# Kernel tuning notes

Measured on AMD Instinct MI355X. Metric: run time of the kernel, lower is better.

Reference implementation:

```python
import jax, jax.numpy as jnp
import numpy as np

EPS = 1e-6  # config.eps


def setup_inputs() -> dict:
    key = jax.random.key(0)
    k1, k2, k3, k4, k5 = jax.random.split(key, 5)
    B, Lq, Lk, D, Dc = 4, 2048, 4096, 1024, 512
    # scale so Poincare-ball norms stay < 1 (realistic hyperbolic embeddings)
    q = jax.random.normal(k1, (B, Lq, D), dtype=jnp.float32) * 0.01
    k_compressed = jax.random.randint(k2, (B, Lk, Dc), 0, 16, dtype=jnp.int32)  # 4-bit codes
    # up-projection weight, torch Linear layout (out=D, in=Dc)
    W_up = jax.random.normal(k3, (D, Dc), dtype=jnp.float32) / np.sqrt(Dc)
    k_scale = jax.random.uniform(k4, (B, Lk, 1), dtype=jnp.float32) * 0.005
    k_zero = jax.random.uniform(k5, (B, Lk, 1), dtype=jnp.float32) * 16.0
    return {"q": q, "k_compressed": k_compressed, "W_up": W_up,
            "k_scale": k_scale, "k_zero": k_zero}


def reference(q, k_compressed, W_up, k_scale, k_zero):
    # dequantize: (B, Lk, Dc)
    kc = k_scale * (k_compressed.astype(jnp.float32) - k_zero)
    # decompress: (B, Lk, D)  --  Linear(Dc -> D), y = x @ W_up.T
    k = jnp.einsum('bkc,dc->bkd', kc, W_up)

    q_sq = jnp.sum(q * q, axis=-1)   # (B, Lq) raw squared norms
    k_sq = jnp.sum(k * k, axis=-1)   # (B, Lk)

    # ||q - k||^2 via algebraic expansion (avoids (B,Lq,Lk,D) diff tensor)
    cross = jnp.einsum('bqd,bkd->bqk', q, k)                 # (B, Lq, Lk)
    diff_norm_sq = jnp.maximum(q_sq[:, :, None] + k_sq[:, None, :] - 2.0 * cross, 0.0)

    # clamped norms used in the Poincare denominator
    q_cl = jnp.minimum(q_sq, 1.0 - EPS)
    k_cl = jnp.minimum(k_sq, 1.0 - EPS)
    denom = (1.0 - q_cl)[:, :, None] * (1.0 - k_cl)[:, None, :] + EPS

    dist = jnp.arccosh(1.0 + 2.0 * diff_norm_sq / denom)     # (B, Lq, Lk)
    return dist
```

## Files before the change

kernel.cpp:

```cpp
#include <hip/hip_runtime.h>
#include <hip/hip_bf16.h>
#include <stdint.h>

typedef unsigned short u16;

#define B_  4
#define LQ  2048
#define LK  4096
#define D_  1024
#define DC  512
#define EPSF 1e-6f

typedef __bf16 bf16x8 __attribute__((ext_vector_type(8)));
typedef float  f32x4  __attribute__((ext_vector_type(4)));

__device__ __forceinline__ u16 f2bf(float f) {
    uint32_t u = __float_as_uint(f);
    uint32_t r = (u + 0x7FFFu + ((u >> 16) & 1u)) >> 16;
    return (u16)r;
}
__device__ __forceinline__ float bf2f(u16 h) {
    return __uint_as_float(((uint32_t)h) << 16);
}
__device__ __forceinline__ void gload_lds16(const void* g, void* l) {
    __builtin_amdgcn_global_load_lds(
        (const __attribute__((address_space(1))) uint32_t*)g,
        (__attribute__((address_space(3))) uint32_t*)l, 16, 0, 0);
}

#define NB_Q2  2048
#define NB_WT  ((D_ / 64) * (DC / 64))
#define NB_WS  4
#define NB_DQ2 4096

__global__ void prep_all(const float* __restrict__ q, u16* __restrict__ qb,
                         float* __restrict__ qsq,
                         const float* __restrict__ w, u16* __restrict__ wth,
                         u16* __restrict__ wtl, float* __restrict__ partS,
                         const int* __restrict__ kc, const float* __restrict__ scale,
                         const float* __restrict__ zero, u16* __restrict__ codeb,
                         u16* __restrict__ kcb) {
    __shared__ float t[64][65];
    __shared__ float red[4];
    const int bid = blockIdx.x;
    const int tid = threadIdx.x;

    if (bid < NB_Q2) {
        int row = bid * 4 + (tid >> 6);
        int ln = tid & 63;
        const float4* qr = reinterpret_cast<const float4*>(q + (size_t)row * D_);
        ushort4* ob = reinterpret_cast<ushort4*>(qb + (size_t)row * D_);
        float s = 0.f;
        #pragma unroll
        for (int c = 0; c < 4; c++) {
            float4 v = qr[c * 64 + ln];
            ushort4 o;
            o.x = f2bf(v.x); o.y = f2bf(v.y); o.z = f2bf(v.z); o.w = f2bf(v.w);
            ob[c * 64 + ln] = o;
            s += v.x * v.x + v.y * v.y + v.z * v.z + v.w * v.w;
        }
        #pragma unroll
        for (int off = 32; off; off >>= 1) s += __shfl_down(s, off);
        if (ln == 0) qsq[row] = s;
    } else if (bid < NB_Q2 + NB_WT) {
        int b2 = bid - NB_Q2;
        int d0 = (b2 % (D_ / 64)) * 64, c0 = (b2 / (D_ / 64)) * 64;
        int tx = tid & 15, ty = tid >> 4;
        #pragma unroll
        for (int r = 0; r < 4; r++) {
            float4 v = *reinterpret_cast<const float4*>(&w[(size_t)(d0 + ty + r * 16) * DC + c0 + tx * 4]);
            t[ty + r * 16][tx * 4 + 0] = v.x;
            t[ty + r * 16][tx * 4 + 1] = v.y;
            t[ty + r * 16][tx * 4 + 2] = v.z;
            t[ty + r * 16][tx * 4 + 3] = v.w;
        }
        __syncthreads();
        #pragma unroll
        for (int r = 0; r < 4; r++) {
            int c = c0 + ty + r * 16;
            ushort4 h, l;
            float v0 = t[tx * 4 + 0][ty + r * 16];
            float v1 = t[tx * 4 + 1][ty + r * 16];
            float v2 = t[tx * 4 + 2][ty + r * 16];
            float v3 = t[tx * 4 + 3][ty + r * 16];
            h.x = f2bf(v0); l.x = f2bf(v0 - bf2f(h.x));
            h.y = f2bf(v1); l.y = f2bf(v1 - bf2f(h.y));
            h.z = f2bf(v2); l.z = f2bf(v2 - bf2f(h.z));
            h.w = f2bf(v3); l.w = f2bf(v3 - bf2f(h.w));
            *reinterpret_cast<ushort4*>(&wth[(size_t)c * D_ + d0 + tx * 4]) = h;
            *reinterpret_cast<ushort4*>(&wtl[(size_t)c * D_ + d0 + tx * 4]) = l;
        }
    } else if (bid < NB_Q2 + NB_WT + NB_WS) {
        int b2 = bid - NB_Q2 - NB_WT;
        int d = b2 * 256 + tid;
        const float4* row = reinterpret_cast<const float4*>(w + (size_t)d * DC);
        float u = 0.f;
        #pragma unroll 8
        for (int i = 0; i < DC / 4; i++) { float4 v = row[i]; u += v.x + v.y + v.z + v.w; }
        float p = u * u;
        #pragma unroll
        for (int off = 32; off; off >>= 1) p += __shfl_down(p, off);
        if ((tid & 63) == 0) red[tid >> 6] = p;
        __syncthreads();
        if (tid == 0) partS[b2] = red[0] + red[1] + red[2] + red[3];
    } else {
        int row = (bid - NB_Q2 - NB_WT - NB_WS) * 4 + (tid >> 6);
        int ln = tid & 63;
        float sc = scale[row], z = zero[row];
        const int2* src = reinterpret_cast<const int2*>(kc + (size_t)row * DC);
        ushort2* dc = reinterpret_cast<ushort2*>(codeb + (size_t)row * DC);
        ushort2* dk = reinterpret_cast<ushort2*>(kcb + (size_t)row * DC);
        #pragma unroll
        for (int c = 0; c < 4; c++) {
            int2 v = src[c * 64 + ln];
            ushort2 cb, kb;
            cb.x = f2bf((float)v.x);
            cb.y = f2bf((float)v.y);
            kb.x = f2bf(sc * ((float)v.x - z));
            kb.y = f2bf(sc * ((float)v.y - z));
            dc[c * 64 + ln] = cb;
            dk[c * 64 + ln] = kb;
        }
    }
}

__global__ __launch_bounds__(256, 2) void gemm_gq(const u16* __restrict__ Wth,
                                                  const u16* __restrict__ Wtl,
                                                  float* __restrict__ gp,
                                                  const u16* __restrict__ Q,
                                                  u16* __restrict__ Cq) {
    __shared__ u16 smem[4][128 * 32];
    const int tid = threadIdx.x;
    const int wid = tid >> 6, lane = tid & 63;
    const int lr = lane & 15, lk = lane >> 4;
    const int wr = wid >> 1, wc = wid & 1;
    const int srow = tid >> 2;
    const int scol = (tid & 3) * 8;

    if (blockIdx.x < 64) {
        const int t = blockIdx.x >> 2, s = blockIdx.x & 3;
        const int m0 = (t & 3) * 128, n0 = (t >> 2) * 128;
        const int K = D_;
        f32x4 acc[4][4] = {};
        const size_t gA = (size_t)(m0 + srow) * K + scol;
        const size_t gB = (size_t)(n0 + srow) * K + scol;
        char* ashb = (char*)(&smem[0][0]) + (wid << 10);
        char* aslb = (char*)(&smem[1][0]) + (wid << 10);
        char* bshb = (char*)(&smem[2][0]) + (wid << 10);
        char* bslb = (char*)(&smem[3][0]) + (wid << 10);

        for (int k0 = s * 256; k0 < s * 256 + 256; k0 += 32) {
            gload_lds16(Wth + gA + k0, ashb);
            gload_lds16(Wth + gA + k0 + (size_t)64 * K, ashb + 4096);
            gload_lds16(Wtl + gA + k0, aslb);
            gload_lds16(Wtl + gA + k0 + (size_t)64 * K, aslb + 4096);
            gload_lds16(Wth + gB + k0, bshb);
            gload_lds16(Wth + gB + k0 + (size_t)64 * K, bshb + 4096);
            gload_lds16(Wtl + gB + k0, bslb);
            gload_lds16(Wtl + gB + k0 + (size_t)64 * K, bslb + 4096);
            __syncthreads();
            bf16x8 afh[4], afl[4], bfh[4], bfl[4];
            #pragma unroll
            for (int i = 0; i < 4; i++) {
                int off = (wr * 64 + i * 16 + lr) * 32 + lk * 8;
                afh[i] = *reinterpret_cast<const bf16x8*>(&smem[0][off]);
                afl[i] = *reinterpret_cast<const bf16x8*>(&smem[1][off]);
            }
            #pragma unroll
            for (int j = 0; j < 4; j++) {
                int off = (wc * 64 + j * 16 + lr) * 32 + lk * 8;
                bfh[j] = *reinterpret_cast<const bf16x8*>(&smem[2][off]);
                bfl[j] = *reinterpret_cast<const bf16x8*>(&smem[3][off]);
            }
            #pragma unroll
            for (int i = 0; i < 4; i++)
                #pragma unroll
                for (int j = 0; j < 4; j++) {
                    acc[i][j] = __builtin_amdgcn_mfma_f32_16x16x32_bf16(afh[i], bfh[j], acc[i][j], 0, 0, 0);
                    acc[i][j] = __builtin_amdgcn_mfma_f32_16x16x32_bf16(afh[i], bfl[j], acc[i][j], 0, 0, 0);
                    acc[i][j] = __builtin_amdgcn_mfma_f32_16x16x32_bf16(afl[i], bfh[j], acc[i][j], 0, 0, 0);
                }
            __syncthreads();
        }
        float* dst = gp + (size_t)s * (DC * DC);
        #pragma unroll
        for (int i = 0; i < 4; i++) {
            int row = m0 + wr * 64 + i * 16 + lk * 4;
            #pragma unroll
            for (int j = 0; j < 4; j++) {
                int col = n0 + wc * 64 + j * 16 + lr;
                #pragma unroll
                for (int r = 0; r < 4; r++)
                    dst[(size_t)(row + r) * DC + col] = acc[i][j][r];
            }
        }
    } else {
        const int q2 = blockIdx.x - 64;
        const int m0 = (q2 & 63) * 128, n0 = (q2 >> 6) * 128;
        const int K = D_;
        const int NT = K / 32;
        f32x4 acc[4][4] = {};
        const u16* ag = Q + (size_t)(m0 + srow) * K + scol;
        const u16* bg = Wth + (size_t)(n0 + srow) * K + scol;

        #define STAGE_P(buf, kt) do {                                          \
            char* asb_ = (char*)(&smem[(buf)][0]) + (wid << 10);               \
            char* bsb_ = (char*)(&smem[2 + (buf)][0]) + (wid << 10);           \
            int k0_ = (kt) * 32;                                               \
            gload_lds16(ag + k0_, asb_);                                       \
            gload_lds16(ag + k0_ + (size_t)64 * K, asb_ + 4096);               \
            gload_lds16(bg + k0_, bsb_);                                       \
            gload_lds16(bg + k0_ + (size_t)64 * K, bsb_ + 4096);               \
        } while (0)

        #define COMPUTE_P(buf) do {                                            \
            bf16x8 af[4], bfr[4];                                              \
            _Pragma("unroll")                                                  \
            for (int i = 0; i < 4; i++)                                        \
                af[i] = *reinterpret_cast<const bf16x8*>(                      \
                    &smem[(buf)][(wr * 64 + i * 16 + lr) * 32 + lk * 8]);      \
            _Pragma("unroll")                                                  \
            for (int j = 0; j < 4; j++)                                        \
                bfr[j] = *reinterpret_cast<const bf16x8*>(                     \
                    &smem[2 + (buf)][(wc * 64 + j * 16 + lr) * 32 + lk * 8]);  \
            asm volatile("s_waitcnt lgkmcnt(0)" ::: "memory");                 \
            __builtin_amdgcn_sched_barrier(0);                                 \
            _Pragma("unroll")                                                  \
            for (int i = 0; i < 4; i++)                                        \
                _Pragma("unroll")                                              \
                for (int j = 0; j < 4; j++)                                    \
                    acc[i][j] = __builtin_amdgcn_mfma_f32_16x16x32_bf16(       \
                        af[i], bfr[j], acc[i][j], 0, 0, 0);                    \
        } while (0)

        STAGE_P(0, 0);
        asm volatile("s_waitcnt vmcnt(0)" ::: "memory");
        __builtin_amdgcn_s_barrier();
        int cur = 0;
        for (int t = 0; t < NT - 1; ++t) {
            STAGE_P(cur ^ 1, t + 1);
            COMPUTE_P(cur);
            asm volatile("s_waitcnt vmcnt(0)" ::: "memory");
            __builtin_amdgcn_s_barrier();
            cur ^= 1;
        }
        COMPUTE_P(cur);
        #undef STAGE_P
        #undef COMPUTE_P

        #pragma unroll
        for (int i = 0; i < 4; i++) {
            int row = m0 + wr * 64 + i * 16 + lk * 4;
            #pragma unroll
            for (int j = 0; j < 4; j++) {
                int col = n0 + wc * 64 + j * 16 + lr;
                #pragma unroll
                for (int r = 0; r < 4; r++)
                    Cq[(size_t)(row + r) * DC + col] = f2bf(acc[i][j][r]);
            }
        }
    }
}

__global__ void g_reduce(const float* __restrict__ gp, u16* __restrict__ Gh,
                         u16* __restrict__ Gl) {
    int i = (blockIdx.x * 256 + threadIdx.x) * 4;
    float4 a = *reinterpret_cast<const float4*>(gp + i);
    float4 b = *reinterpret_cast<const float4*>(gp + (DC * DC) + i);
    float4 c = *reinterpret_cast<const float4*>(gp + 2 * (DC * DC) + i);
    float4 d = *reinterpret_cast<const float4*>(gp + 3 * (DC * DC) + i);
    float v0 = a.x + b.x + c.x + d.x;
    float v1 = a.y + b.y + c.y + d.y;
    float v2 = a.z + b.z + c.z + d.z;
    float v3 = a.w + b.w + c.w + d.w;
    ushort4 h, l;
    h.x = f2bf(v0); l.x = f2bf(v0 - bf2f(h.x));
    h.y = f2bf(v1); l.y = f2bf(v1 - bf2f(h.y));
    h.z = f2bf(v2); l.z = f2bf(v2 - bf2f(h.z));
    h.w = f2bf(v3); l.w = f2bf(v3 - bf2f(h.w));
    *reinterpret_cast<ushort4*>(Gh + i) = h;
    *reinterpret_cast<ushort4*>(Gl + i) = l;
}

__global__ __launch_bounds__(256, 2) void gemm_ksq(const u16* __restrict__ A,
                                                   const u16* __restrict__ Bh,
                                                   const u16* __restrict__ Bl,
                                                   float* __restrict__ part1,
                                                   float* __restrict__ part2) {
    __shared__ u16 As[3][128 * 32];
    __shared__ u16 Bsh[3][128 * 32];
    __shared__ u16 Bsl[3][128 * 32];
    const int wg = (blockIdx.x & 7) * 64 + (blockIdx.x >> 3);
    const int m0 = (wg & 127) * 128, n0 = (wg >> 7) * 128;
    const int tid = threadIdx.x;
    const int wid = tid >> 6, lane = tid & 63;
    const int lr = lane & 15, lk = lane >> 4;
    const int wr = wid >> 1, wc = wid & 1;
    const int K = DC;
    const int NT = K / 32;

    f32x4 acc[4][4] = {};
    const int srow = tid >> 2;
    const int scol = (tid & 3) * 8;
    const u16* ag = A + (size_t)(m0 + srow) * K + scol;
    const u16* bhg = Bh + (size_t)(n0 + srow) * K + scol;
    const u16* blg = Bl + (size_t)(n0 + srow) * K + scol;

    #define STAGE_K(buf, kt) do {                                          \
        char* asb_  = (char*)(&As[(buf)][0]) + (wid << 10);                \
        char* bshb_ = (char*)(&Bsh[(buf)][0]) + (wid << 10);               \
        char* bslb_ = (char*)(&Bsl[(buf)][0]) + (wid << 10);               \
        int k0_ = (kt) * 32;                                               \
        gload_lds16(ag + k0_, asb_);                                       \
        gload_lds16(ag + k0_ + (size_t)64 * K, asb_ + 4096);               \
        gload_lds16(bhg + k0_, bshb_);                                     \
        gload_lds16(bhg + k0_ + (size_t)64 * K, bshb_ + 4096);             \
        gload_lds16(blg + k0_, bslb_);                                     \
        gload_lds16(blg + k0_ + (size_t)64 * K, bslb_ + 4096);             \
    } while (0)

    #define COMPUTE_K(buf) do {                                            \
        bf16x8 af[4], bh_[4], bl_[4];                                      \
        _Pragma("unroll")                                                  \
        for (int i = 0; i < 4; i++)                                        \
            af[i] = *reinterpret_cast<const bf16x8*>(                      \
                &As[(buf)][(wr * 64 + i * 16 + lr) * 32 + lk * 8]);        \
        _Pragma("unroll")                                                  \
        for (int j = 0; j < 4; j++) {                                      \
            int off = (wc * 64 + j * 16 + lr) * 32 + lk * 8;               \
            bh_[j] = *reinterpret_cast<const bf16x8*>(&Bsh[(buf)][off]);   \
            bl_[j] = *reinterpret_cast<const bf16x8*>(&Bsl[(buf)][off]);   \
        }                                                                  \
        asm volatile("s_waitcnt lgkmcnt(0)" ::: "memory");                 \
        __builtin_amdgcn_sched_barrier(0);                                 \
        _Pragma("unroll")                                                  \
        for (int i = 0; i < 4; i++)                                        \
            _Pragma("unroll")                                              \
            for (int j = 0; j < 4; j++) {                                  \
                acc[i][j] = __builtin_amdgcn_mfma_f32_16x16x32_bf16(       \
                    af[i], bh_[j], acc[i][j], 0, 0, 0);                    \
                acc[i][j] = __builtin_amdgcn_mfma_f32_16x16x32_bf16(       \
                    af[i], bl_[j], acc[i][j], 0, 0, 0);                    \
            }                                                              \
    } while (0)

    STAGE_K(0, 0);
    STAGE_K(1, 1);
    asm volatile("s_waitcnt vmcnt(6)" ::: "memory");
    __builtin_amdgcn_s_barrier();
    int cur = 0;
    for (int t = 0; t < NT - 2; ++t) {
        int nx = cur + 2; if (nx >= 3) nx -= 3;
        STAGE_K(nx, t + 2);
        COMPUTE_K(cur);
        asm volatile("s_waitcnt vmcnt(6)" ::: "memory");
        __builtin_amdgcn_s_barrier();
        cur = (cur + 1 == 3) ? 0 : cur + 1;
    }
    COMPUTE_K(cur);
    asm volatile("s_waitcnt vmcnt(0)" ::: "memory");
    __builtin_amdgcn_s_barrier();
    cur = (cur + 1 == 3) ? 0 : cur + 1;
    COMPUTE_K(cur);
    #undef STAGE_K
    #undef COMPUTE_K

    #pragma unroll
    for (int i = 0; i < 4; i++) {
        #pragma unroll
        for (int r = 0; r < 4; r++) {
            int row = m0 + wr * 64 + i * 16 + lk * 4 + r;
            float p1 = 0.f, p2 = 0.f;
            #pragma unroll
            for (int j = 0; j < 4; j++) {
                int col = n0 + wc * 64 + j * 16 + lr;
                float cg = acc[i][j][r];
                float cd = bf2f(A[(size_t)row * DC + col]);
                p1 = fmaf(cg, cd, p1);
                p2 += cg;
            }
            #pragma unroll
            for (int m = 1; m <= 8; m <<= 1) {
                p1 += __shfl_xor(p1, m);
                p2 += __shfl_xor(p2, m);
            }
            if (lr == 0) {
                size_t idx = (size_t)row * 8 + (wg >> 7) * 2 + wc;
                part1[idx] = p1;
                part2[idx] = p2;
            }
        }
    }
}

__global__ __launch_bounds__(256, 2) void gemm_dist2(const u16* __restrict__ Qp,
                                                     const u16* __restrict__ Kc,
                                                     const float* __restrict__ qsq,
                                                     const float* __restrict__ part1,
                                                     const float* __restrict__ part2,
                                                     const float* __restrict__ partS,
                                                     const float* __restrict__ kscale,
                                                     const float* __restrict__ kzero,
                                                     float* __restrict__ out) {
    const int wgid = (blockIdx.x & 7) * 256 + (blockIdx.x >> 3);
    const int bx = wgid & 15, by = (wgid >> 4) & 31, bz = wgid >> 9;

    const u16* A  = Qp + (size_t)bz * LQ * DC;
    const u16* Bt = Kc + (size_t)bz * LK * DC;
    float* O = out + (size_t)bz * LQ * LK;
    const float* qs_ = qsq + bz * LQ;

    __shared__ u16 As[3][128 * 32];
    __shared__ u16 Bs[3][128 * 32];
    __shared__ float kss[128];
    const int tid = threadIdx.x;
    const int wid = tid >> 6, lane = tid & 63;
    const int lr = lane & 15, lk = lane >> 4;
    const int wr = wid >> 1, wc = wid & 1;
    const int m0 = bx * 128, n0 = by * 128;
    const int K = DC;
    const int NT = K / 32;

    if (tid < 128) {
        int gcol = bz * LK + n0 + tid;
        const float4* p1 = reinterpret_cast<const float4*>(part1 + (size_t)gcol * 8);
        const float4* p2 = reinterpret_cast<const float4*>(part2 + (size_t)gcol * 8);
        float4 a0 = p1[0], a1 = p1[1];
        float4 b0 = p2[0], b1 = p2[1];
        float P1 = a0.x + a0.y + a0.z + a0.w + a1.x + a1.y + a1.z + a1.w;
        float P2 = b0.x + b0.y + b0.z + b0.w + b1.x + b1.y + b1.z + b1.w;
        float S = partS[0] + partS[1] + partS[2] + partS[3];
        float sc = kscale[gcol], z = kzero[gcol];
        kss[tid] = sc * sc * (P1 - 2.f * z * P2 + z * z * S);
    }

    f32x4 acc[4][4] = {};
    const int srow = tid >> 2;
    const int scol = (tid & 3) * 8;
    const u16* ag = A + (size_t)(m0 + srow) * K + scol;
    const u16* bg = Bt + (size_t)(n0 + srow) * K + scol;

    #define STAGE_D(buf, kt) do {                                          \
        char* asb_ = (char*)(&As[(buf)][0]) + (wid << 10);                 \
        char* bsb_ = (char*)(&Bs[(buf)][0]) + (wid << 10);                 \
        int k0_ = (kt) * 32;                                               \
        gload_lds16(ag + k0_, asb_);                                       \
        gload_lds16(ag + k0_ + (size_t)64 * K, asb_ + 4096);               \
        gload_lds16(bg + k0_, bsb_);                                       \
        gload_lds16(bg + k0_ + (size_t)64 * K, bsb_ + 4096);               \
    } while (0)

    #define COMPUTE_D(buf) do {                                            \
        bf16x8 af[4], bfr[4];                                              \
        _Pragma("unroll")                                                  \
        for (int i = 0; i < 4; i++)                                        \
            af[i] = *reinterpret_cast<const bf16x8*>(                      \
                &As[(buf)][(wr * 64 + i * 16 + lr) * 32 + lk * 8]);        \
        _Pragma("unroll")                                                  \
        for (int j = 0; j < 4; j++)                                        \
            bfr[j] = *reinterpret_cast<const bf16x8*>(                     \
                &Bs[(buf)][(wc * 64 + j * 16 + lr) * 32 + lk * 8]);        \
        asm volatile("s_waitcnt lgkmcnt(0)" ::: "memory");                 \
        __builtin_amdgcn_sched_barrier(0);                                 \
        _Pragma("unroll")                                                  \
        for (int i = 0; i < 4; i++)                                        \
            _Pragma("unroll")                                              \
            for (int j = 0; j < 4; j++)                                    \
                acc[i][j] = __builtin_amdgcn_mfma_f32_16x16x32_bf16(       \
                    af[i], bfr[j], acc[i][j], 0, 0, 0);                    \
    } while (0)

    STAGE_D(0, 0);
    STAGE_D(1, 1);
    asm volatile("s_waitcnt vmcnt(4)" ::: "memory");
    __builtin_amdgcn_s_barrier();
    int cur = 0;
    for (int t = 0; t < NT - 2; ++t) {
        int nx = cur + 2; if (nx >= 3) nx -= 3;
        STAGE_D(nx, t + 2);
        COMPUTE_D(cur);
        asm volatile("s_waitcnt vmcnt(4)" ::: "memory");
        __builtin_amdgcn_s_barrier();
        cur = (cur + 1 == 3) ? 0 : cur + 1;
    }
    COMPUTE_D(cur);
    asm volatile("s_waitcnt vmcnt(0)" ::: "memory");
    __builtin_amdgcn_s_barrier();
    cur = (cur + 1 == 3) ? 0 : cur + 1;
    COMPUTE_D(cur);
    #undef STAGE_D
    #undef COMPUTE_D

    const float LN2 = 0.69314718055994531f;
    float ksv[4], pkv[4];
    #pragma unroll
    for (int j = 0; j < 4; j++) {
        ksv[j] = kss[wc * 64 + j * 16 + lr];
        pkv[j] = 1.f - fminf(ksv[j], 1.f - EPSF);
    }
    #pragma unroll
    for (int i = 0; i < 4; i++) {
        int row = m0 + wr * 64 + i * 16 + lk * 4;
        #pragma unroll
        for (int r = 0; r < 4; r++) {
            int gr = row + r;
            float qs = qs_[gr];
            float pq = 1.f - fminf(qs, 1.f - EPSF);
            float* orow = O + (size_t)gr * LK + n0 + wc * 64 + lr;
            #pragma unroll
            for (int j = 0; j < 4; j++) {
                float d = fmaxf(fmaf(acc[i][j][r], -2.f, qs + ksv[j]), 0.f);
                float den = fmaf(pq, pkv[j], EPSF);
                float u = (d + d) * __builtin_amdgcn_rcpf(den);
                float s = __builtin_amdgcn_sqrtf(u * (u + 2.f));
                orow[j * 16] = LN2 * __builtin_amdgcn_logf(1.f + u + s);
            }
        }
    }
}

extern "C" void kernel_launch(void* const* d_in, const int* in_sizes, int n_in,
                              void* d_out, int out_size, void* d_ws, size_t ws_size,
                              hipStream_t stream) {
    const float* q      = (const float*)d_in[0];
    const int*   kcmp   = (const int*)d_in[1];
    const float* wup    = (const float*)d_in[2];
    const float* kscale = (const float*)d_in[3];
    const float* kzero  = (const float*)d_in[4];
    float* out = (float*)d_out;

    char* ws = (char*)d_ws;
    u16*   qb    = (u16*)(ws);
    u16*   qp    = (u16*)(ws + 16777216);
    u16*   codeb = (u16*)(ws + 25165824);
    u16*   kcb   = (u16*)(ws + 41943040);
    u16*   wth   = (u16*)(ws + 58720256);
    u16*   wtl   = (u16*)(ws + 59768832);
    u16*   gh    = (u16*)(ws + 60817408);
    u16*   gl    = (u16*)(ws + 61341696);
    float* qsq   = (float*)(ws + 61865984);
    float* part1 = (float*)(ws + 61898752);
    float* part2 = (float*)(ws + 62423040);
    float* partS = (float*)(ws + 62947328);
    float* gp    = (float*)(ws + 62947344);

    prep_all<<<NB_Q2 + NB_WT + NB_WS + NB_DQ2, 256, 0, stream>>>(
        q, qb, qsq, wup, wth, wtl, partS, kcmp, kscale, kzero, codeb, kcb);

    gemm_gq<<<64 + 256, 256, 0, stream>>>(wth, wtl, gp, qb, qp);

    g_reduce<<<DC * DC / 1024, 256, 0, stream>>>(gp, gh, gl);

    gemm_ksq<<<512, 256, 0, stream>>>(codeb, gh, gl, part1, part2);

    gemm_dist2<<<2048, 256, 0, stream>>>(qp, kcb, qsq, part1, part2, partS,
                                         kscale, kzero, out);
}
```

Measured before the change: 138.5 us.

## Fuse q bf16 conversion and norms into projection GEMM, drop split-K gram reduce

The q float-to-bf16 conversion and squared-norm computation move out of the prep kernel and into the Q-projection GEMM, which now loads fp32 q directly, converts it in registers and writes it to LDS. The W Gram-matrix GEMM no longer uses a 4-way split-K with a separate reduce kernel; 16 blocks each run the full K loop and emit hi/lo bf16 directly. This removes the bf16 q round trip through memory, one kernel launch and the partial-sum buffer. In exchange, the A operand is loaded synchronously through registers instead of async global-to-LDS, and the Gram GEMM has only 16 blocks doing longer serial work.

Result: slower. 149.4 us (+7.9%).

```diff
diff --git a/kernel.cpp b/kernel.cpp
--- a/kernel.cpp
+++ b/kernel.cpp
@@ -28,14 +28,11 @@
         (__attribute__((address_space(3))) uint32_t*)l, 16, 0, 0);
 }
 
-#define NB_Q2  2048
 #define NB_WT  ((D_ / 64) * (DC / 64))
 #define NB_WS  4
 #define NB_DQ2 4096
 
-__global__ void prep_all(const float* __restrict__ q, u16* __restrict__ qb,
-                         float* __restrict__ qsq,
-                         const float* __restrict__ w, u16* __restrict__ wth,
+__global__ void prep_all(const float* __restrict__ w, u16* __restrict__ wth,
                          u16* __restrict__ wtl, float* __restrict__ partS,
                          const int* __restrict__ kc, const float* __restrict__ scale,
                          const float* __restrict__ zero, u16* __restrict__ codeb,
@@ -45,25 +42,8 @@
     const int bid = blockIdx.x;
     const int tid = threadIdx.x;
 
-    if (bid < NB_Q2) {
-        int row = bid * 4 + (tid >> 6);
-        int ln = tid & 63;
-        const float4* qr = reinterpret_cast<const float4*>(q + (size_t)row * D_);
-        ushort4* ob = reinterpret_cast<ushort4*>(qb + (size_t)row * D_);
-        float s = 0.f;
-        #pragma unroll
-        for (int c = 0; c < 4; c++) {
-            float4 v = qr[c * 64 + ln];
-            ushort4 o;
-            o.x = f2bf(v.x); o.y = f2bf(v.y); o.z = f2bf(v.z); o.w = f2bf(v.w);
-            ob[c * 64 + ln] = o;
-            s += v.x * v.x + v.y * v.y + v.z * v.z + v.w * v.w;
-        }
-        #pragma unroll
-        for (int off = 32; off; off >>= 1) s += __shfl_down(s, off);
-        if (ln == 0) qsq[row] = s;
-    } else if (bid < NB_Q2 + NB_WT) {
-        int b2 = bid - NB_Q2;
+    if (bid < NB_WT) {
+        int b2 = bid;
         int d0 = (b2 % (D_ / 64)) * 64, c0 = (b2 / (D_ / 64)) * 64;
         int tx = tid & 15, ty = tid >> 4;
         #pragma unroll
@@ -90,8 +70,8 @@
             *reinterpret_cast<ushort4*>(&wth[(size_t)c * D_ + d0 + tx * 4]) = h;
             *reinterpret_cast<ushort4*>(&wtl[(size_t)c * D_ + d0 + tx * 4]) = l;
         }
-    } else if (bid < NB_Q2 + NB_WT + NB_WS) {
-        int b2 = bid - NB_Q2 - NB_WT;
+    } else if (bid < NB_WT + NB_WS) {
+        int b2 = bid - NB_WT;
         int d = b2 * 256 + tid;
         const float4* row = reinterpret_cast<const float4*>(w + (size_t)d * DC);
         float u = 0.f;
@@ -104,7 +84,7 @@
         __syncthreads();
         if (tid == 0) partS[b2] = red[0] + red[1] + red[2] + red[3];
     } else {
-        int row = (bid - NB_Q2 - NB_WT - NB_WS) * 4 + (tid >> 6);
+        int row = (bid - NB_WT - NB_WS) * 4 + (tid >> 6);
         int ln = tid & 63;
         float sc = scale[row], z = zero[row];
         const int2* src = reinterpret_cast<const int2*>(kc + (size_t)row * DC);
@@ -126,9 +106,11 @@
 
 __global__ __launch_bounds__(256, 2) void gemm_gq(const u16* __restrict__ Wth,
                                                   const u16* __restrict__ Wtl,
-                                                  float* __restrict__ gp,
-                                                  const u16* __restrict__ Q,
-                                                  u16* __restrict__ Cq) {
+                                                  u16* __restrict__ Gh,
+                                                  u16* __restrict__ Gl,
+                                                  const float* __restrict__ Qf,
+                                                  u16* __restrict__ Cq,
+                                                  float* __restrict__ qsq) {
     __shared__ u16 smem[4][128 * 32];
     const int tid = threadIdx.x;
     const int wid = tid >> 6, lane = tid & 63;
@@ -137,9 +119,8 @@
     const int srow = tid >> 2;
     const int scol = (tid & 3) * 8;
 
-    if (blockIdx.x < 64) {
-        const int t = blockIdx.x >> 2, s = blockIdx.x & 3;
-        const int m0 = (t & 3) * 128, n0 = (t >> 2) * 128;
+    if (blockIdx.x < 16) {
+        const int m0 = (blockIdx.x & 3) * 128, n0 = (blockIdx.x >> 2) * 128;
         const int K = D_;
         f32x4 acc[4][4] = {};
         const size_t gA = (size_t)(m0 + srow) * K + scol;
@@ -149,7 +130,7 @@
         char* bshb = (char*)(&smem[2][0]) + (wid << 10);
         char* bslb = (char*)(&smem[3][0]) + (wid << 10);
 
-        for (int k0 = s * 256; k0 < s * 256 + 256; k0 += 32) {
+        for (int k0 = 0; k0 < K; k0 += 32) {
             gload_lds16(Wth + gA + k0, ashb);
             gload_lds16(Wth + gA + k0 + (size_t)64 * K, ashb + 4096);
             gload_lds16(Wtl + gA + k0, aslb);
@@ -182,7 +163,6 @@
                 }
             __syncthreads();
         }
-        float* dst = gp + (size_t)s * (DC * DC);
         #pragma unroll
         for (int i = 0; i < 4; i++) {
             int row = m0 + wr * 64 + i * 16 + lk * 4;
@@ -190,27 +170,54 @@
             for (int j = 0; j < 4; j++) {
                 int col = n0 + wc * 64 + j * 16 + lr;
                 #pragma unroll
-                for (int r = 0; r < 4; r++)
-                    dst[(size_t)(row + r) * DC + col] = acc[i][j][r];
+                for (int r = 0; r < 4; r++) {
+                    float v = acc[i][j][r];
+                    u16 h = f2bf(v);
+                    Gh[(size_t)(row + r) * DC + col] = h;
+                    Gl[(size_t)(row + r) * DC + col] = f2bf(v - bf2f(h));
+                }
             }
         }
     } else {
-        const int q2 = blockIdx.x - 64;
+        const int q2 = blockIdx.x - 16;
         const int m0 = (q2 & 63) * 128, n0 = (q2 >> 6) * 128;
         const int K = D_;
         const int NT = K / 32;
         f32x4 acc[4][4] = {};
-        const u16* ag = Q + (size_t)(m0 + srow) * K + scol;
+        const float* aq = Qf + (size_t)(m0 + srow) * K + (tid & 3) * 8;
         const u16* bg = Wth + (size_t)(n0 + srow) * K + scol;
-
-        #define STAGE_P(buf, kt) do {                                          \
-            char* asb_ = (char*)(&smem[(buf)][0]) + (wid << 10);               \
+        float sq0 = 0.f, sq1 = 0.f;
+        float4 a0, a1, a2, a3;
+
+        #define LOADA(kt) do {                                                 \
+            const float4* p0 = reinterpret_cast<const float4*>(aq + (kt) * 32);\
+            const float4* p1 = reinterpret_cast<const float4*>(                \
+                aq + (size_t)64 * K + (kt) * 32);                              \
+            a0 = p0[0]; a1 = p0[1]; a2 = p1[0]; a3 = p1[1];                    \
+        } while (0)
+
+        #define WRITEA(buf) do {                                               \
+            bf16x8 v0, v1;                                                     \
+            v0[0] = (__bf16)a0.x; v0[1] = (__bf16)a0.y;                        \
+            v0[2] = (__bf16)a0.z; v0[3] = (__bf16)a0.w;                        \
+            v0[4] = (__bf16)a1.x; v0[5] = (__bf16)a1.y;                        \
+            v0[6] = (__bf16)a1.z; v0[7] = (__bf16)a1.w;                        \
+            v1[0] = (__bf16)a2.x; v1[1] = (__bf16)a2.y;                        \
+            v1[2] = (__bf16)a2.z; v1[3] = (__bf16)a2.w;                        \
+            v1[4] = (__bf16)a3.x; v1[5] = (__bf16)a3.y;                        \
+            v1[6] = (__bf16)a3.z; v1[7] = (__bf16)a3.w;                        \
+            *reinterpret_cast<bf16x8*>(&smem[(buf)][wid * 512 + lane * 8]) = v0; \
+            *reinterpret_cast<bf16x8*>(&smem[(buf)][wid * 512 + lane * 8 + 2048]) = v1; \
+            sq0 += a0.x * a0.x + a0.y * a0.y + a0.z * a0.z + a0.w * a0.w       \
+                 + a1.x * a1.x + a1.y * a1.y + a1.z * a1.z + a1.w * a1.w;      \
+            sq1 += a2.x * a2.x + a2.y * a2.y + a2.z * a2.z + a2.w * a2.w       \
+                 + a3.x * a3.x + a3.y * a3.y + a3.z * a3.z + a3.w * a3.w;      \
+        } while (0)
+
+        #define STAGEB(buf, kt) do {                                           \
             char* bsb_ = (char*)(&smem[2 + (buf)][0]) + (wid << 10);           \
-            int k0_ = (kt) * 32;                                               \
-            gload_lds16(ag + k0_, asb_);                                       \
-            gload_lds16(ag + k0_ + (size_t)64 * K, asb_ + 4096);               \
-            gload_lds16(bg + k0_, bsb_);                                       \
-            gload_lds16(bg + k0_ + (size_t)64 * K, bsb_ + 4096);               \
+            gload_lds16(bg + (kt) * 32, bsb_);                                 \
+            gload_lds16(bg + (kt) * 32 + (size_t)64 * K, bsb_ + 4096);         \
         } while (0)
 
         #define COMPUTE_P(buf) do {                                            \
@@ -233,20 +240,31 @@
                         af[i], bfr[j], acc[i][j], 0, 0, 0);                    \
         } while (0)
 
-        STAGE_P(0, 0);
-        asm volatile("s_waitcnt vmcnt(0)" ::: "memory");
-        __builtin_amdgcn_s_barrier();
+        LOADA(0);
+        STAGEB(0, 0);
+        WRITEA(0);
+        __syncthreads();
         int cur = 0;
         for (int t = 0; t < NT - 1; ++t) {
-            STAGE_P(cur ^ 1, t + 1);
+            LOADA(t + 1);
+            STAGEB(cur ^ 1, t + 1);
             COMPUTE_P(cur);
-            asm volatile("s_waitcnt vmcnt(0)" ::: "memory");
-            __builtin_amdgcn_s_barrier();
+            WRITEA(cur ^ 1);
+            __syncthreads();
             cur ^= 1;
         }
         COMPUTE_P(cur);
-        #undef STAGE_P
+        #undef LOADA
+        #undef WRITEA
+        #undef STAGEB
         #undef COMPUTE_P
+
+        sq0 += __shfl_xor(sq0, 1); sq0 += __shfl_xor(sq0, 2);
+        sq1 += __shfl_xor(sq1, 1); sq1 += __shfl_xor(sq1, 2);
+        if ((tid & 3) == 0 && q2 < 64) {
+            qsq[m0 + srow] = sq0;
+            qsq[m0 + 64 + srow] = sq1;
+        }
 
         #pragma unroll
         for (int i = 0; i < 4; i++) {
@@ -260,26 +278,6 @@
             }
         }
     }
-}
-
-__global__ void g_reduce(const float* __restrict__ gp, u16* __restrict__ Gh,
-                         u16* __restrict__ Gl) {
-    int i = (blockIdx.x * 256 + threadIdx.x) * 4;
-    float4 a = *reinterpret_cast<const float4*>(gp + i);
-    float4 b = *reinterpret_cast<const float4*>(gp + (DC * DC) + i);
-    float4 c = *reinterpret_cast<const float4*>(gp + 2 * (DC * DC) + i);
-    float4 d = *reinterpret_cast<const float4*>(gp + 3 * (DC * DC) + i);
-    float v0 = a.x + b.x + c.x + d.x;
-    float v1 = a.y + b.y + c.y + d.y;
-    float v2 = a.z + b.z + c.z + d.z;
-    float v3 = a.w + b.w + c.w + d.w;
-    ushort4 h, l;
-    h.x = f2bf(v0); l.x = f2bf(v0 - bf2f(h.x));
-    h.y = f2bf(v1); l.y = f2bf(v1 - bf2f(h.y));
-    h.z = f2bf(v2); l.z = f2bf(v2 - bf2f(h.z));
-    h.w = f2bf(v3); l.w = f2bf(v3 - bf2f(h.w));
-    *reinterpret_cast<ushort4*>(Gh + i) = h;
-    *reinterpret_cast<ushort4*>(Gl + i) = l;
 }
 
 __global__ __launch_bounds__(256, 2) void gemm_ksq(const u16* __restrict__ A,
@@ -530,26 +528,22 @@
     float* out = (float*)d_out;
 
     char* ws = (char*)d_ws;
-    u16*   qb    = (u16*)(ws);
-    u16*   qp    = (u16*)(ws + 16777216);
-    u16*   codeb = (u16*)(ws + 25165824);
-    u16*   kcb   = (u16*)(ws + 41943040);
-    u16*   wth   = (u16*)(ws + 58720256);
-    u16*   wtl   = (u16*)(ws + 59768832);
-    u16*   gh    = (u16*)(ws + 60817408);
-    u16*   gl    = (u16*)(ws + 61341696);
-    float* qsq   = (float*)(ws + 61865984);
-    float* part1 = (float*)(ws + 61898752);
-    float* part2 = (float*)(ws + 62423040);
-    float* partS = (float*)(ws + 62947328);
-    float* gp    = (float*)(ws + 62947344);
-
-    prep_all<<<NB_Q2 + NB_WT + NB_WS + NB_DQ2, 256, 0, stream>>>(
-        q, qb, qsq, wup, wth, wtl, partS, kcmp, kscale, kzero, codeb, kcb);
-
-    gemm_gq<<<64 + 256, 256, 0, stream>>>(wth, wtl, gp, qb, qp);
-
-    g_reduce<<<DC * DC / 1024, 256, 0, stream>>>(gp, gh, gl);
+    u16*   qp    = (u16*)(ws);
+    u16*   codeb = (u16*)(ws + 8388608);
+    u16*   kcb   = (u16*)(ws + 25165824);
+    u16*   wth   = (u16*)(ws + 41943040);
+    u16*   wtl   = (u16*)(ws + 42991616);
+    u16*   gh    = (u16*)(ws + 44040192);
+    u16*   gl    = (u16*)(ws + 44564480);
+    float* qsq   = (float*)(ws + 45088768);
+    float* part1 = (float*)(ws + 45121536);
+    float* part2 = (float*)(ws + 45645824);
+    float* partS = (float*)(ws + 46170112);
+
+    prep_all<<<NB_WT + NB_WS + NB_DQ2, 256, 0, stream>>>(
+        wup, wth, wtl, partS, kcmp, kscale, kzero, codeb, kcb);
+
+    gemm_gq<<<16 + 256, 256, 0, stream>>>(wth, wtl, gh, gl, q, qp, qsq);
 
     gemm_ksq<<<512, 256, 0, stream>>>(codeb, gh, gl, part1, part2);
 
```
